# Performance work log

Measured on AMD Instinct MI355X. Metric: run time of the kernel, lower is better.

Reference implementation:

```python
import jax, jax.numpy as jnp
import numpy as np

N, D, K = 131072, 512, 1024


def setup_inputs() -> dict:
    key = jax.random.key(0)
    k1, k2 = jax.random.split(key)
    features = jax.random.normal(k1, (N, D), dtype=jnp.float32)
    centroids = jax.random.normal(k2, (D, K), dtype=jnp.float32)
    return {"features": features, "centroids": centroids}


def reference(features, centroids):
    # Squared Euclidean distance via norm expansion (avoids [N, D, K] broadcast):
    x_sq = jnp.sum(features * features, axis=1, keepdims=True)      # [N, 1]
    c_sq = jnp.sum(centroids * centroids, axis=0, keepdims=True)    # [1, K]
    cross = jnp.einsum('nd,dk->nk', features, centroids)            # [N, K]
    distances = x_sq - 2.0 * cross + c_sq                           # [N, K]
    assignments = jnp.argmin(distances, axis=-1)                    # [N]
    return assignments[:, None].astype(jnp.float32)                 # [N, 1]
```

## Files before the change

### kernel.cpp

```cpp
#include <hip/hip_runtime.h>
#include <hip/hip_bf16.h>

#define NPTS 131072
#define DIMS 512
#define KC   1024

typedef _Float16 f16;
using f16x8  = __attribute__((ext_vector_type(8))) _Float16;
using f32x16 = __attribute__((ext_vector_type(16))) float;
typedef unsigned short u16;
typedef unsigned int u32;
typedef unsigned long long u64;

#define CT_OFF     0ull
#define CSQ_OFF    1048576ull
#define CSQP_OFF   1052672ull
#define CNT_OFF    1118208ull
#define LIST_OFF   1118464ull
#define WS_NEEDED  1642752ull

#define MARGIN 0.2f

__device__ __forceinline__ u32 f2o(float f) {
    u32 u = __float_as_uint(f);
    return (u & 0x80000000u) ? ~u : (u | 0x80000000u);
}
__device__ __forceinline__ float o2f(u32 o) {
    u32 u = (o & 0x80000000u) ? (o & 0x7FFFFFFFu) : ~o;
    return __uint_as_float(u);
}
__device__ __forceinline__ u64 umin64(u64 a, u64 b) { return a < b ? a : b; }
__device__ __forceinline__ u64 umax64(u64 a, u64 b) { return a > b ? a : b; }

__device__ __forceinline__ void async_load16(const void* g, const void* l) {
    auto gp = reinterpret_cast<__attribute__((address_space(1))) void*>(
        reinterpret_cast<uintptr_t>(g));
    auto lp = reinterpret_cast<__attribute__((address_space(3))) void*>(
        (unsigned int)reinterpret_cast<uintptr_t>(l));
    __builtin_amdgcn_global_load_lds(gp, lp, 16, 0, 0);
}

__global__ void split_c_kernel(const float* __restrict__ C,
                               u16* __restrict__ ct, float* __restrict__ csq_part) {
    __shared__ float t[32][33];
    int bn = blockIdx.x, bd = blockIdx.y;
    int tx = threadIdx.x & 31, ty = threadIdx.x >> 5;
#pragma unroll
    for (int r = 0; r < 32; r += 8)
        t[ty + r][tx] = C[(size_t)(bd * 32 + ty + r) * KC + bn * 32 + tx];
    __syncthreads();
#pragma unroll
    for (int r = 0; r < 32; r += 8) {
        int n = bn * 32 + ty + r, d = bd * 32 + tx;
        float v = t[tx][ty + r];
        f16 h = (f16)v;
        ct[(size_t)n * DIMS + d] = *reinterpret_cast<u16*>(&h);
        float sq = v * v;
#pragma unroll
        for (int m = 1; m < 32; m <<= 1)
            sq += __shfl_xor(sq, m, 64);
        if (tx == 0) csq_part[bd * KC + n] = sq;
    }
}

__global__ void csq_reduce_kernel(const float* __restrict__ part, float* __restrict__ csq) {
    int k = blockIdx.x * 256 + threadIdx.x;
    float s = 0.f;
#pragma unroll
    for (int p = 0; p < 16; ++p) s += part[p * KC + k];
    csq[k] = s;
}

__global__ void csq_kernel(const float* __restrict__ C, float* __restrict__ csq) {
    int k = blockIdx.x * blockDim.x + threadIdx.x;
    if (k < KC) {
        float s = 0.f;
        for (int d = 0; d < DIMS; ++d) {
            float v = C[d * KC + k];
            s = fmaf(v, v, s);
        }
        csq[k] = s;
    }
}

__global__ __launch_bounds__(256, 4) void gemm_argmin_kernel(
    const float* __restrict__ F, const u16* __restrict__ Ct,
    const float* __restrict__ csq, float* __restrict__ out,
    u32* __restrict__ cnt, u32* __restrict__ list)
{
    __shared__ __align__(16) uint8_t smem[16384];
    __shared__ float csq_l[1024];
    __shared__ u32 lcnt, lbase;
    __shared__ u32 lrows[128];

    const int tid  = threadIdx.x;
    const int lane = tid & 63;
    const int wid  = tid >> 6;
    const int wm   = wid >> 1, wn = wid & 1;
    const int py   = (int)blockIdx.x;

    for (int i = tid; i < 1024; i += 256) csq_l[i] = csq[i];
    if (tid == 0) lcnt = 0;

    const int brow = tid >> 1, bh_ = tid & 1;
    const float* bF = F + (size_t)(py * 128 + brow) * DIMS + bh_ * 16;
    const int bxr = (brow >> 1) & 3;
    const unsigned bw0 = 8192u + (unsigned)(brow * 64 + (((bh_ * 2 + 0) ^ bxr) * 16));
    const unsigned bw1 = 8192u + (unsigned)(brow * 64 + (((bh_ * 2 + 1) ^ bxr) * 16));

    const int c_st = (lane & 3) ^ ((lane >> 3) & 3);
    const u16* aBase0 = Ct + (size_t)(wid * 32 + (lane >> 2)) * DIMS + c_st * 8;
    const unsigned aw = (unsigned)(wid * 32) * 64;

    const int kh = lane >> 5;
    const int cl = lane & 31;
    const int xr = (cl >> 1) & 3;
    const unsigned mb = (unsigned)cl * 64;
    const unsigned offs0 = mb + (unsigned)(((0 + kh) ^ xr) * 16);
    const unsigned offs1 = mb + (unsigned)(((2 + kh) ^ xr) * 16);

    u64 bestA[2] = {~0ull, ~0ull};
    u64 bestB[2] = {~0ull, ~0ull};

    for (int cx = 0; cx < 8; ++cx) {
        const u16* aBase = aBase0 + (size_t)(cx * 128) * DIMS;

        f32x16 acc[2][2];
#pragma unroll
        for (int i = 0; i < 2; ++i)
#pragma unroll
            for (int j = 0; j < 2; ++j)
#pragma unroll
                for (int e = 0; e < 16; ++e) acc[i][j][e] = 0.f;

        for (int kt = 0; kt < DIMS / 32; ++kt) {
            const int k0 = kt * 32;
            float4 f0 = *(const float4*)(bF + k0);
            float4 f1 = *(const float4*)(bF + k0 + 4);
            float4 f2 = *(const float4*)(bF + k0 + 8);
            float4 f3 = *(const float4*)(bF + k0 + 12);

            __syncthreads();
            async_load16(aBase + k0,             smem + aw);
            async_load16(aBase + 16 * DIMS + k0, smem + aw + 1024);
            {
                float v[16] = {f0.x, f0.y, f0.z, f0.w, f1.x, f1.y, f1.z, f1.w,
                               f2.x, f2.y, f2.z, f2.w, f3.x, f3.y, f3.z, f3.w};
                f16x8 h0, h1;
#pragma unroll
                for (int i = 0; i < 8; ++i) h0[i] = (f16)v[i];
#pragma unroll
                for (int i = 0; i < 8; ++i) h1[i] = (f16)v[8 + i];
                *(f16x8*)(smem + bw0) = h0;
                *(f16x8*)(smem + bw1) = h1;
            }
            __syncthreads();

#pragma unroll
            for (int s = 0; s < 2; ++s) {
                const unsigned off = s ? offs1 : offs0;
                f16x8 a[2], b[2];
#pragma unroll
                for (int mt = 0; mt < 2; ++mt)
                    a[mt] = *(const f16x8*)(smem + wm * 4096 + mt * 2048 + off);
#pragma unroll
                for (int nt = 0; nt < 2; ++nt)
                    b[nt] = *(const f16x8*)(smem + 8192 + wn * 4096 + nt * 2048 + off);
#pragma unroll
                for (int mt = 0; mt < 2; ++mt)
#pragma unroll
                    for (int nt = 0; nt < 2; ++nt)
                        acc[mt][nt] = __builtin_amdgcn_mfma_f32_32x32x16_f16(a[mt], b[nt], acc[mt][nt], 0, 0, 0);
            }
        }

#pragma unroll
        for (int nt = 0; nt < 2; ++nt)
#pragma unroll
            for (int mt = 0; mt < 2; ++mt)
#pragma unroll
                for (int reg = 0; reg < 16; ++reg) {
                    const int rl = wm * 64 + mt * 32 + (reg & 3) + 8 * (reg >> 2) + 4 * kh;
                    const float d = fmaf(-2.0f, acc[mt][nt][reg], csq_l[cx * 128 + rl]);
                    const u64 key = ((u64)f2o(d) << 32) | (u32)(cx * 128 + rl);
                    const u64 t = umin64(bestA[nt], key);
                    bestB[nt] = umin64(bestB[nt], umax64(bestA[nt], key));
                    bestA[nt] = t;
                }
    }

    __syncthreads();
    u64* tbl = (u64*)smem;

#pragma unroll
    for (int nt = 0; nt < 2; ++nt) {
        const u64 a = bestA[nt], b = bestB[nt];
        const u64 oa = __shfl_xor(a, 32, 64);
        const u64 ob = __shfl_xor(b, 32, 64);
        const u64 lo = umin64(a, oa);
        const u64 bb = umin64(umax64(a, oa), umin64(b, ob));
        if (kh == 0) {
            const int p = wn * 64 + nt * 32 + cl;
            tbl[(p * 2 + wm) * 2 + 0] = lo;
            tbl[(p * 2 + wm) * 2 + 1] = bb;
        }
    }
    __syncthreads();

    if (tid < 128) {
        const u64 a0 = tbl[tid * 4 + 0], b0 = tbl[tid * 4 + 1];
        const u64 a1 = tbl[tid * 4 + 2], b1 = tbl[tid * 4 + 3];
        const u64 m1 = umin64(a0, a1);
        const u64 m2 = umin64(umax64(a0, a1), umin64(b0, b1));
        const int row = py * 128 + tid;
        const float d1 = o2f((u32)(m1 >> 32));
        const float d2 = o2f((u32)(m2 >> 32));
        if (d2 - d1 > MARGIN) {
            out[row] = (float)(u32)(m1 & 1023u);
        } else {
            u32 li = atomicAdd(&lcnt, 1u);
            lrows[li] = (u32)row;
        }
    }
    __syncthreads();
    if (tid == 0 && lcnt > 0) lbase = atomicAdd(cnt, lcnt);
    __syncthreads();
    if (tid < lcnt) list[lbase + tid] = lrows[tid];
}

__global__ __launch_bounds__(256) void rescue2_kernel(
    const float* __restrict__ F, const float* __restrict__ C,
    const float* __restrict__ csq, const u32* __restrict__ cnt,
    const u32* __restrict__ list, u32* __restrict__ wptr, float* __restrict__ out)
{
    __shared__ float xs[4][512];
    __shared__ u64 wavemin[4][4];
    __shared__ int rows_s[4];

    const int tid = threadIdx.x;
    const int lane = tid & 63;
    const int wid = tid >> 6;
    const u32 n = cnt[0];

    for (;;) {
        __syncthreads();
        u32 base;
        if (tid == 0) {
            base = atomicAdd(wptr, 4u);
            rows_s[0] = (int)base;
        }
        __syncthreads();
        base = (u32)rows_s[0];
        if (base >= n) break;

        int rows[4];
#pragma unroll
        for (int j = 0; j < 4; ++j) {
            u32 idx = base + j;
            rows[j] = (int)list[idx < n ? idx : (n - 1)];
        }
#pragma unroll
        for (int j = 0; j < 4; ++j) {
            if (tid < 128)
                *(float4*)&xs[j][tid * 4] = *(const float4*)&F[(size_t)rows[j] * DIMS + tid * 4];
        }
        __syncthreads();

        float dot[4][4];
#pragma unroll
        for (int j = 0; j < 4; ++j)
#pragma unroll
            for (int q = 0; q < 4; ++q) dot[j][q] = 0.f;

#pragma unroll 4
        for (int d = 0; d < DIMS; ++d) {
            float cv[4];
#pragma unroll
            for (int q = 0; q < 4; ++q) cv[q] = C[d * KC + tid + 256 * q];
            float xv[4];
#pragma unroll
            for (int j = 0; j < 4; ++j) xv[j] = xs[j][d];
#pragma unroll
            for (int j = 0; j < 4; ++j)
#pragma unroll
                for (int q = 0; q < 4; ++q)
                    dot[j][q] = fmaf(xv[j], cv[q], dot[j][q]);
        }

#pragma unroll
        for (int j = 0; j < 4; ++j) {
            u64 best = ~0ull;
#pragma unroll
            for (int q = 0; q < 4; ++q) {
                const int k = tid + 256 * q;
                const float dist = csq[k] - 2.0f * dot[j][q];
                best = umin64(best, ((u64)f2o(dist) << 32) | (u32)k);
            }
#pragma unroll
            for (int off = 32; off > 0; off >>= 1)
                best = umin64(best, __shfl_xor(best, off, 64));
            if (lane == 0) wavemin[j][wid] = best;
        }
        __syncthreads();
        if (tid < 4) {
            const u32 idx = base + tid;
            if (idx < n) {
                u64 b = umin64(umin64(wavemin[tid][0], wavemin[tid][1]),
                               umin64(wavemin[tid][2], wavemin[tid][3]));
                out[list[idx]] = (float)(u32)(b & 0xFFFFFFFFull);
            }
        }
    }
}

__global__ __launch_bounds__(256, 3) void assign_kernel_fp32(
    const float* __restrict__ F, const float* __restrict__ C,
    const float* __restrict__ csq, float* __restrict__ out)
{
    __shared__ float At[32][68];
    __shared__ float Bs[32 * 256];
    __shared__ u64 best_row[64];

    const int tid = threadIdx.x;
    const int tx = tid & 31;
    const int ty = tid >> 5;
    const int n0 = blockIdx.x * 64;

    if (tid < 64) best_row[tid] = ~0ull;

    u64 best[8];
#pragma unroll
    for (int r = 0; r < 8; ++r) best[r] = ~0ull;

    const int arow = tid >> 3;
    const int ac4  = tid & 7;
    const float* Atp = &At[0][ty * 8];
    const float* Bsp = &Bs[tx * 4];

    for (int kt = 0; kt < 4; ++kt) {
        float acc[8][8];
#pragma unroll
        for (int r = 0; r < 8; ++r)
#pragma unroll
            for (int j = 0; j < 8; ++j) acc[r][j] = 0.f;

        for (int dt = 0; dt < DIMS / 32; ++dt) {
            __syncthreads();
#pragma unroll
            for (int i = 0; i < 2; ++i) {
                int row = arow + 32 * i;
                float4 av = *(const float4*)&F[(long)(n0 + row) * DIMS + dt * 32 + ac4 * 4];
                At[ac4 * 4 + 0][row] = av.x;
                At[ac4 * 4 + 1][row] = av.y;
                At[ac4 * 4 + 2][row] = av.z;
                At[ac4 * 4 + 3][row] = av.w;
            }
#pragma unroll
            for (int i = 0; i < 8; ++i) {
                int idx = tid + 256 * i;
                int d  = idx >> 6;
                int c4 = idx & 63;
                float4 bv = *(const float4*)&C[(long)(dt * 32 + d) * KC + kt * 256 + c4 * 4];
                *(float4*)&Bs[d * 256 + c4 * 4] = bv;
            }
            __syncthreads();

#pragma unroll 8
            for (int dd = 0; dd < 32; ++dd) {
                float4 a0 = *(const float4*)(Atp + dd * 68);
                float4 a1 = *(const float4*)(Atp + dd * 68 + 4);
                float4 b0 = *(const float4*)(Bsp + dd * 256);
                float4 b1 = *(const float4*)(Bsp + dd * 256 + 128);
                float a[8] = {a0.x, a0.y, a0.z, a0.w, a1.x, a1.y, a1.z, a1.w};
                float bb[8] = {b0.x, b0.y, b0.z, b0.w, b1.x, b1.y, b1.z, b1.w};
#pragma unroll
                for (int r = 0; r < 8; ++r)
#pragma unroll
                    for (int j = 0; j < 8; ++j)
                        acc[r][j] = fmaf(a[r], bb[j], acc[r][j]);
            }
        }

        float4 cs0 = *(const float4*)&csq[kt * 256 + tx * 4];
        float4 cs1 = *(const float4*)&csq[kt * 256 + 128 + tx * 4];
        float cs[8] = {cs0.x, cs0.y, cs0.z, cs0.w, cs1.x, cs1.y, cs1.z, cs1.w};
#pragma unroll
        for (int j = 0; j < 8; ++j) {
            int k = kt * 256 + ((j < 4) ? (tx * 4 + j) : (128 + tx * 4 + (j - 4)));
#pragma unroll
            for (int r = 0; r < 8; ++r) {
                float val = cs[j] - 2.0f * acc[r][j];
                u64 key = ((u64)f2o(val) << 32) | (u64)(unsigned)k;
                if (key < best[r]) best[r] = key;
            }
        }
    }

#pragma unroll
    for (int r = 0; r < 8; ++r)
        atomicMin(&best_row[ty * 8 + r], best[r]);
    __syncthreads();

    if (tid < 64)
        out[n0 + tid] = (float)(unsigned)(best_row[tid] & 0xFFFFFFFFull);
}

extern "C" void kernel_launch(void* const* d_in, const int* in_sizes, int n_in,
                              void* d_out, int out_size, void* d_ws, size_t ws_size,
                              hipStream_t stream) {
    const float* F = (const float*)d_in[0];
    const float* C = (const float*)d_in[1];
    float* out = (float*)d_out;
    char* ws = (char*)d_ws;

    if (ws_size < WS_NEEDED) {
        float* csq = (float*)d_ws;
        csq_kernel<<<KC / 256, 256, 0, stream>>>(C, csq);
        assign_kernel_fp32<<<NPTS / 64, 256, 0, stream>>>(F, C, csq, out);
        return;
    }

    u16* Ct = (u16*)(ws + CT_OFF);
    float* csq  = (float*)(ws + CSQ_OFF);
    float* csqp = (float*)(ws + CSQP_OFF);
    u32* cnt  = (u32*)(ws + CNT_OFF);
    u32* list = (u32*)(ws + LIST_OFF);

    hipMemsetAsync(cnt, 0, 8, stream);
    split_c_kernel<<<dim3(KC / 32, DIMS / 32), 256, 0, stream>>>(C, Ct, csqp);
    csq_reduce_kernel<<<KC / 256, 256, 0, stream>>>(csqp, csq);
    gemm_argmin_kernel<<<NPTS / 128, 256, 0, stream>>>(F, Ct, csq, out, cnt, list);
    rescue2_kernel<<<1024, 256, 0, stream>>>(F, C, csq, cnt, list, cnt + 1, out);
}
```

Baseline: 729.0 us.

## Keep feature tile in registers and double-buffer centroid tiles with 512 threads

```diff
diff --git a/kernel.cpp b/kernel.cpp
--- a/kernel.cpp
+++ b/kernel.cpp
@@ -83,7 +83,7 @@
     }
 }
 
-__global__ __launch_bounds__(256, 4) void gemm_argmin_kernel(
+__global__ __launch_bounds__(512, 2) void gemm_argmin_kernel(
     const float* __restrict__ F, const u16* __restrict__ Ct,
     const float* __restrict__ csq, float* __restrict__ out,
     u32* __restrict__ cnt, u32* __restrict__ list)
@@ -96,111 +96,91 @@
     const int tid  = threadIdx.x;
     const int lane = tid & 63;
     const int wid  = tid >> 6;
-    const int wm   = wid >> 1, wn = wid & 1;
+    const int wm   = wid >> 2;
+    const int wn   = wid & 3;
     const int py   = (int)blockIdx.x;
-
-    for (int i = tid; i < 1024; i += 256) csq_l[i] = csq[i];
-    if (tid == 0) lcnt = 0;
-
-    const int brow = tid >> 1, bh_ = tid & 1;
-    const float* bF = F + (size_t)(py * 128 + brow) * DIMS + bh_ * 16;
-    const int bxr = (brow >> 1) & 3;
-    const unsigned bw0 = 8192u + (unsigned)(brow * 64 + (((bh_ * 2 + 0) ^ bxr) * 16));
-    const unsigned bw1 = 8192u + (unsigned)(brow * 64 + (((bh_ * 2 + 1) ^ bxr) * 16));
-
-    const int c_st = (lane & 3) ^ ((lane >> 3) & 3);
-    const u16* aBase0 = Ct + (size_t)(wid * 32 + (lane >> 2)) * DIMS + c_st * 8;
-    const unsigned aw = (unsigned)(wid * 32) * 64;
 
     const int kh = lane >> 5;
     const int cl = lane & 31;
+
+    for (int i = tid; i < 1024; i += 512) csq_l[i] = csq[i];
+    if (tid == 0) lcnt = 0;
+
+    const float* fRow = F + (size_t)(py * 128 + wn * 32 + cl) * DIMS + kh * 8;
+    f16x8 b_reg[32];
+#pragma unroll
+    for (int kt = 0; kt < 16; ++kt)
+#pragma unroll
+        for (int s = 0; s < 2; ++s) {
+            float4 x0 = *(const float4*)(fRow + kt * 32 + s * 16);
+            float4 x1 = *(const float4*)(fRow + kt * 32 + s * 16 + 4);
+            f16x8 h;
+            h[0] = (f16)x0.x; h[1] = (f16)x0.y; h[2] = (f16)x0.z; h[3] = (f16)x0.w;
+            h[4] = (f16)x1.x; h[5] = (f16)x1.y; h[6] = (f16)x1.z; h[7] = (f16)x1.w;
+            b_reg[kt * 2 + s] = h;
+        }
+
+    const int lr   = lane >> 2;
+    const int c_st = (lane & 3) ^ ((lane >> 3) & 3);
+    const u16* aStage = Ct + (size_t)(wid * 16 + lr) * DIMS + c_st * 8;
+    const unsigned awdst = (unsigned)(wid * 1024);
+
     const int xr = (cl >> 1) & 3;
-    const unsigned mb = (unsigned)cl * 64;
-    const unsigned offs0 = mb + (unsigned)(((0 + kh) ^ xr) * 16);
-    const unsigned offs1 = mb + (unsigned)(((2 + kh) ^ xr) * 16);
-
-    u64 bestA[2] = {~0ull, ~0ull};
-    u64 bestB[2] = {~0ull, ~0ull};
+    const unsigned mbase = (unsigned)cl * 64;
+    const unsigned offs[2] = { mbase + (unsigned)(((0 + kh) ^ xr) * 16),
+                               mbase + (unsigned)(((2 + kh) ^ xr) * 16) };
+
+    u64 bestA = ~0ull, bestB = ~0ull;
+    f32x16 acc[2];
+
+    async_load16(aStage, smem + awdst);
+    __syncthreads();
 
     for (int cx = 0; cx < 8; ++cx) {
-        const u16* aBase = aBase0 + (size_t)(cx * 128) * DIMS;
-
-        f32x16 acc[2][2];
-#pragma unroll
-        for (int i = 0; i < 2; ++i)
-#pragma unroll
-            for (int j = 0; j < 2; ++j)
-#pragma unroll
-                for (int e = 0; e < 16; ++e) acc[i][j][e] = 0.f;
-
-        for (int kt = 0; kt < DIMS / 32; ++kt) {
-            const int k0 = kt * 32;
-            float4 f0 = *(const float4*)(bF + k0);
-            float4 f1 = *(const float4*)(bF + k0 + 4);
-            float4 f2 = *(const float4*)(bF + k0 + 8);
-            float4 f3 = *(const float4*)(bF + k0 + 12);
-
+        const size_t cxoff = (size_t)cx * (128 * DIMS);
+#pragma unroll
+        for (int e = 0; e < 16; ++e) { acc[0][e] = 0.f; acc[1][e] = 0.f; }
+
+#pragma unroll
+        for (int kt = 0; kt < 16; ++kt) {
+            if (!(cx == 7 && kt == 15)) {
+                const size_t noff = (kt == 15) ? (cxoff + (size_t)(128 * DIMS))
+                                               : (cxoff + (size_t)((kt + 1) * 32));
+                async_load16(aStage + noff,
+                             smem + (((kt + 1) & 1) ? 8192u : 0u) + awdst);
+            }
+            const unsigned buf = (kt & 1) ? 8192u : 0u;
+#pragma unroll
+            for (int s = 0; s < 2; ++s) {
+                f16x8 a0 = *(const f16x8*)(smem + buf + wm * 4096 + 0 * 2048 + offs[s]);
+                f16x8 a1 = *(const f16x8*)(smem + buf + wm * 4096 + 1 * 2048 + offs[s]);
+                acc[0] = __builtin_amdgcn_mfma_f32_32x32x16_f16(a0, b_reg[kt * 2 + s], acc[0], 0, 0, 0);
+                acc[1] = __builtin_amdgcn_mfma_f32_32x32x16_f16(a1, b_reg[kt * 2 + s], acc[1], 0, 0, 0);
+            }
             __syncthreads();
-            async_load16(aBase + k0,             smem + aw);
-            async_load16(aBase + 16 * DIMS + k0, smem + aw + 1024);
-            {
-                float v[16] = {f0.x, f0.y, f0.z, f0.w, f1.x, f1.y, f1.z, f1.w,
-                               f2.x, f2.y, f2.z, f2.w, f3.x, f3.y, f3.z, f3.w};
-                f16x8 h0, h1;
-#pragma unroll
-                for (int i = 0; i < 8; ++i) h0[i] = (f16)v[i];
-#pragma unroll
-                for (int i = 0; i < 8; ++i) h1[i] = (f16)v[8 + i];
-                *(f16x8*)(smem + bw0) = h0;
-                *(f16x8*)(smem + bw1) = h1;
-            }
-            __syncthreads();
-
-#pragma unroll
-            for (int s = 0; s < 2; ++s) {
-                const unsigned off = s ? offs1 : offs0;
-                f16x8 a[2], b[2];
-#pragma unroll
-                for (int mt = 0; mt < 2; ++mt)
-                    a[mt] = *(const f16x8*)(smem + wm * 4096 + mt * 2048 + off);
-#pragma unroll
-                for (int nt = 0; nt < 2; ++nt)
-                    b[nt] = *(const f16x8*)(smem + 8192 + wn * 4096 + nt * 2048 + off);
-#pragma unroll
-                for (int mt = 0; mt < 2; ++mt)
-#pragma unroll
-                    for (int nt = 0; nt < 2; ++nt)
-                        acc[mt][nt] = __builtin_amdgcn_mfma_f32_32x32x16_f16(a[mt], b[nt], acc[mt][nt], 0, 0, 0);
-            }
-        }
-
-#pragma unroll
-        for (int nt = 0; nt < 2; ++nt)
-#pragma unroll
-            for (int mt = 0; mt < 2; ++mt)
-#pragma unroll
-                for (int reg = 0; reg < 16; ++reg) {
-                    const int rl = wm * 64 + mt * 32 + (reg & 3) + 8 * (reg >> 2) + 4 * kh;
-                    const float d = fmaf(-2.0f, acc[mt][nt][reg], csq_l[cx * 128 + rl]);
-                    const u64 key = ((u64)f2o(d) << 32) | (u32)(cx * 128 + rl);
-                    const u64 t = umin64(bestA[nt], key);
-                    bestB[nt] = umin64(bestB[nt], umax64(bestA[nt], key));
-                    bestA[nt] = t;
-                }
-    }
-
-    __syncthreads();
-    u64* tbl = (u64*)smem;
-
-#pragma unroll
-    for (int nt = 0; nt < 2; ++nt) {
-        const u64 a = bestA[nt], b = bestB[nt];
-        const u64 oa = __shfl_xor(a, 32, 64);
-        const u64 ob = __shfl_xor(b, 32, 64);
-        const u64 lo = umin64(a, oa);
-        const u64 bb = umin64(umax64(a, oa), umin64(b, ob));
+        }
+
+#pragma unroll
+        for (int mt = 0; mt < 2; ++mt)
+#pragma unroll
+            for (int reg = 0; reg < 16; ++reg) {
+                const int rl = wm * 64 + mt * 32 + (reg & 3) + 8 * (reg >> 2) + 4 * kh;
+                const float d = fmaf(-2.0f, acc[mt][reg], csq_l[cx * 128 + rl]);
+                const u64 key = ((u64)f2o(d) << 32) | (u32)(cx * 128 + rl);
+                const u64 t = umin64(bestA, key);
+                bestB = umin64(bestB, umax64(bestA, key));
+                bestA = t;
+            }
+    }
+
+    {
+        const u64 oa = __shfl_xor(bestA, 32, 64);
+        const u64 ob = __shfl_xor(bestB, 32, 64);
+        const u64 lo = umin64(bestA, oa);
+        const u64 bb = umin64(umax64(bestA, oa), umin64(bestB, ob));
+        u64* tbl = (u64*)smem;
         if (kh == 0) {
-            const int p = wn * 64 + nt * 32 + cl;
+            const int p = wn * 32 + cl;
             tbl[(p * 2 + wm) * 2 + 0] = lo;
             tbl[(p * 2 + wm) * 2 + 1] = bb;
         }
@@ -208,6 +188,7 @@
     __syncthreads();
 
     if (tid < 128) {
+        u64* tbl = (u64*)smem;
         const u64 a0 = tbl[tid * 4 + 0], b0 = tbl[tid * 4 + 1];
         const u64 a1 = tbl[tid * 4 + 2], b1 = tbl[tid * 4 + 3];
         const u64 m1 = umin64(a0, a1);
@@ -429,6 +410,6 @@
     hipMemsetAsync(cnt, 0, 8, stream);
     split_c_kernel<<<dim3(KC / 32, DIMS / 32), 256, 0, stream>>>(C, Ct, csqp);
     csq_reduce_kernel<<<KC / 256, 256, 0, stream>>>(csqp, csq);
-    gemm_argmin_kernel<<<NPTS / 128, 256, 0, stream>>>(F, Ct, csq, out, cnt, list);
+    gemm_argmin_kernel<<<NPTS / 128, 512, 0, stream>>>(F, Ct, csq, out, cnt, list);
     rescue2_kernel<<<1024, 256, 0, stream>>>(F, C, csq, cnt, list, cnt + 1, out);
 }
```

After: 691.2 us. -5.2%, faster.
